# Kernel tuning notes

Measured on AMD Instinct MI355X. Metric: run time of the kernel, lower is better.

Reference implementation:

```python
import jax, jax.numpy as jnp
import numpy as np

B, C, H, N, M = 8, 256, 4, 2048, 2048
D = C // H  # head_dim = 64
EPS = 1e-5


def conv1d(x, W, b):
    # 1x1 Conv1d == per-position GEMM: x [B, Cin, N], W [Cout, Cin], b [Cout]
    return jnp.einsum('oi,bin->bon', W, x) + b[:, None]


def setup_inputs() -> dict:
    key = jax.random.key(0)
    ks = jax.random.split(key, 16)
    s = 1.0 / np.sqrt(C)
    s2 = 1.0 / np.sqrt(2 * C)
    return {
        'desc1': jax.random.normal(ks[0], (B, C, N), jnp.float32),
        'desc2': jax.random.normal(ks[1], (B, C, M), jnp.float32),
        'weight_v': jax.random.uniform(ks[2], (B, M), jnp.float32),
        'Wq': jax.random.normal(ks[3], (C, C), jnp.float32) * s,
        'bq': jnp.zeros((C,), jnp.float32),
        'Wk': jax.random.normal(ks[4], (C, C), jnp.float32) * s,
        'bk': jnp.zeros((C,), jnp.float32),
        'Wv': jax.random.normal(ks[5], (C, C), jnp.float32) * s,
        'bv': jnp.zeros((C,), jnp.float32),
        'Wm': jax.random.normal(ks[6], (C, C), jnp.float32) * s,
        'bm': jnp.zeros((C,), jnp.float32),
        'Wc1': jax.random.normal(ks[7], (2 * C, 2 * C), jnp.float32) * s2,
        'bc1': jnp.zeros((2 * C,), jnp.float32),
        'bn_gamma': jnp.ones((2 * C,), jnp.float32),
        'bn_beta': jnp.zeros((2 * C,), jnp.float32),
        'bn_mean': jnp.zeros((2 * C,), jnp.float32),
        'bn_var': jnp.ones((2 * C,), jnp.float32),
        'Wc2': jax.random.normal(ks[8], (C, 2 * C), jnp.float32) * s2,
        'bc2': jnp.zeros((C,), jnp.float32),
    }


def reference(desc1, desc2, weight_v, Wq, bq, Wk, bk, Wv, bv, Wm, bm,
              Wc1, bc1, bn_gamma, bn_beta, bn_mean, bn_var, Wc2, bc2):
    b = desc1.shape[0]
    # projections -> [B, H, D, N/M]
    q = conv1d(desc1, Wq, bq).reshape(b, H, D, -1)
    k = conv1d(desc2, Wk, bk).reshape(b, H, D, -1)
    v = conv1d(desc2, Wv, bv).reshape(b, H, D, -1)
    v = v * weight_v[:, None, None, :]
    score = jax.nn.softmax(jnp.einsum('bhdn,bhdm->bhnm', q, k) / jnp.sqrt(jnp.asarray(D, q.dtype)), axis=-1)
    add_value = jnp.einsum('bhnm,bhdm->bhdn', score, v).reshape(b, H * D, -1)
    add_value = conv1d(add_value, Wm, bm)
    cat = jnp.concatenate([desc1, add_value], axis=1)  # [B, 2C, N]
    h = conv1d(cat, Wc1, bc1)
    # BatchNorm (inference, running stats)
    inv = bn_gamma / jnp.sqrt(bn_var + EPS)
    h = jax.nn.relu(h * inv[:, None] + (bn_beta - bn_mean * inv)[:, None])
    return desc1 + conv1d(h, Wc2, bc2)
```

## Files before the change

### kernel.cpp

```cpp
#include <hip/hip_runtime.h>
#include <hip/hip_bf16.h>
#include <math.h>

constexpr int Bb = 8;
constexpr int Cc = 256;
constexpr int Hh = 4;
constexpr int Nn = 2048;
constexpr int Mm = 2048;
constexpr size_t BCN = (size_t)Bb * Cc * Nn;

typedef __attribute__((ext_vector_type(8))) short short8;
typedef __attribute__((ext_vector_type(4))) float f32x4;

__device__ __forceinline__ unsigned short bfu(float x) {
  __hip_bfloat16 b = __float2bfloat16(x);
  return __builtin_bit_cast(unsigned short, b);
}

__device__ __forceinline__ void gload16(const unsigned short* g, unsigned short* l) {
  __builtin_amdgcn_global_load_lds(
      (const __attribute__((address_space(1))) unsigned int*)g,
      (__attribute__((address_space(3))) unsigned int*)l, 16, 0, 0);
}

__global__ __launch_bounds__(256) void quantw_kernel(
    const float* __restrict__ s0, const float* __restrict__ s1,
    const float* __restrict__ s2, const float* __restrict__ s3,
    const float* __restrict__ s4, const float* __restrict__ s5,
    unsigned short* __restrict__ d0, unsigned short* __restrict__ d1,
    unsigned short* __restrict__ d2, unsigned short* __restrict__ d3,
    unsigned short* __restrict__ d4, unsigned short* __restrict__ d5)
{
  const int seg = blockIdx.y;
  const float* s; unsigned short* d; int cnt; float sc = 1.f;
  switch (seg) {
    case 0: s = s0; d = d0; cnt = 65536;  sc = 0.125f; break;
    case 1: s = s1; d = d1; cnt = 65536;  break;
    case 2: s = s2; d = d2; cnt = 65536;  break;
    case 3: s = s3; d = d3; cnt = 65536;  break;
    case 4: s = s4; d = d4; cnt = 262144; break;
    default: s = s5; d = d5; cnt = 131072; break;
  }
  for (int i = blockIdx.x * 256 + threadIdx.x; i < cnt / 4; i += 64 * 256) {
    float4 v = ((const float4*)s)[i];
    unsigned int lo = bfu(v.x * sc) | ((unsigned int)bfu(v.y * sc) << 16);
    unsigned int hi = bfu(v.z * sc) | ((unsigned int)bfu(v.w * sc) << 16);
    ((uint2*)d)[i] = make_uint2(lo, hi);
  }
}

__global__ __launch_bounds__(256) void trans_kernel(
    const float* __restrict__ S1, const float* __restrict__ S2,
    unsigned short* __restrict__ D1, unsigned short* __restrict__ D2)
{
  __shared__ float T[64][65];
  const int z = blockIdx.z, b = z & 7;
  const float* S = (z >> 3) ? S2 : S1;
  unsigned short* D = (z >> 3) ? D2 : D1;
  const int n0 = blockIdx.x * 64, c0 = blockIdx.y * 64;
  const int t = threadIdx.x, t4 = t >> 6, tl = t & 63;

  #pragma unroll
  for (int r = 0; r < 16; ++r) {
    int cl = r * 4 + t4;
    T[cl][tl] = S[((size_t)b * 256 + c0 + cl) * 2048 + n0 + tl];
  }
  __syncthreads();
  #pragma unroll
  for (int r = 0; r < 16; ++r) {
    int nl = r * 4 + t4;
    D[((size_t)b * 2048 + n0 + nl) * 256 + c0 + tl] = bfu(T[tl][nl]);
  }
}

template<int K1, int K2, int COUT, int EPI>
__global__ __launch_bounds__(256) void gemm_kernel(
    const unsigned short* __restrict__ Wb,
    const unsigned short* __restrict__ X1, const unsigned short* __restrict__ X2,
    const float* __restrict__ bias,
    const float* __restrict__ p0, const float* __restrict__ p1,
    const float* __restrict__ p2, const float* __restrict__ p3,
    void* __restrict__ Yv, float oscale)
{
  constexpr int KT = K1 + K2;
  constexpr bool TRANS = (EPI == 0 || EPI == 2 || EPI == 3);
  __shared__ unsigned short lds[2 * 128 * 64];
  unsigned short* Wl = lds;
  unsigned short* Xl = lds + 128 * 64;

  const int t = threadIdx.x;
  const int w = t >> 6, l = t & 63;
  const int c = l & 15, h4 = l >> 4;
  const int n0 = blockIdx.x * 128;
  const int o0 = blockIdx.y * 128;
  const int b  = blockIdx.z;
  const int wo = (w & 1) * 64, wn = (w >> 1) * 64;

  const int r8  = t >> 3;
  const int kgx = (t & 7) ^ (r8 & 7);

  const unsigned short* Xb1 = X1 + (size_t)b * 2048 * K1;

  f32x4 acc[4][4] = {};

  #pragma unroll 1
  for (int kt = 0; kt < KT / 64; ++kt) {
    __syncthreads();
    #pragma unroll
    for (int q = 0; q < 4; ++q) {
      int row = q * 32 + r8;
      gload16(Wb + (size_t)(o0 + row) * KT + kt * 64 + kgx * 8,
              Wl + q * 2048 + w * 512);
      const unsigned short* src;
      if constexpr (K2 == 0) {
        src = Xb1 + (size_t)(n0 + row) * K1 + kt * 64 + kgx * 8;
      } else {
        src = (kt * 64 < K1)
          ? Xb1 + (size_t)(n0 + row) * K1 + kt * 64 + kgx * 8
          : X2 + ((size_t)b * 2048 + n0 + row) * K2 + (kt * 64 - K1) + kgx * 8;
      }
      gload16(src, Xl + q * 2048 + w * 512);
    }
    __syncthreads();

    #pragma unroll
    for (int kk = 0; kk < 2; ++kk) {
      short8 wf[4], xf[4];
      #pragma unroll
      for (int f = 0; f < 4; ++f) {
        int row = wo + f * 16 + c;
        wf[f] = *(const short8*)((const char*)Wl + row * 128 + (((kk * 4 + h4) ^ (row & 7)) << 4));
      }
      #pragma unroll
      for (int f = 0; f < 4; ++f) {
        int row = wn + f * 16 + c;
        xf[f] = *(const short8*)((const char*)Xl + row * 128 + (((kk * 4 + h4) ^ (row & 7)) << 4));
      }
      #pragma unroll
      for (int i = 0; i < 4; ++i)
        #pragma unroll
        for (int j = 0; j < 4; ++j) {
          if constexpr (TRANS)
            acc[i][j] = __builtin_amdgcn_mfma_f32_16x16x32_bf16(xf[i], wf[j], acc[i][j], 0, 0, 0);
          else
            acc[i][j] = __builtin_amdgcn_mfma_f32_16x16x32_bf16(wf[i], xf[j], acc[i][j], 0, 0, 0);
        }
    }
  }

  if constexpr (EPI == 0) {
    unsigned short* Y = (unsigned short*)Yv;
    #pragma unroll
    for (int j = 0; j < 4; ++j) {
      int og = o0 + wo + j * 16 + c;
      float bb = bias[og] * oscale;
      int hh = og >> 6, d = og & 63;
      unsigned short* Yp = Y + (((size_t)b * Hh + hh) * 2048) * 64 + d;
      #pragma unroll
      for (int i = 0; i < 4; ++i) {
        #pragma unroll
        for (int r = 0; r < 4; ++r) {
          int ng = n0 + wn + i * 16 + h4 * 4 + r;
          Yp[(size_t)ng * 64] = bfu(acc[i][j][r] + bb);
        }
      }
    }
  } else if constexpr (EPI == 2) {
    unsigned short* Y = (unsigned short*)Yv;
    #pragma unroll
    for (int j = 0; j < 4; ++j) {
      int og = o0 + wo + j * 16 + c;
      float bb = bias[og];
      #pragma unroll
      for (int i = 0; i < 4; ++i)
        #pragma unroll
        for (int r = 0; r < 4; ++r) {
          int ng = n0 + wn + i * 16 + h4 * 4 + r;
          Y[((size_t)b * 2048 + ng) * 256 + og] = bfu(acc[i][j][r] + bb);
        }
    }
  } else if constexpr (EPI == 3) {
    unsigned short* Y = (unsigned short*)Yv;
    #pragma unroll
    for (int j = 0; j < 4; ++j) {
      int og = o0 + wo + j * 16 + c;
      float bb  = bias[og];
      float inv = p0[og] / sqrtf(p3[og] + 1e-5f);
      float add = p1[og] - p2[og] * inv;
      #pragma unroll
      for (int i = 0; i < 4; ++i)
        #pragma unroll
        for (int r = 0; r < 4; ++r) {
          int ng = n0 + wn + i * 16 + h4 * 4 + r;
          float v = fmaxf((acc[i][j][r] + bb) * inv + add, 0.f);
          Y[((size_t)b * 2048 + ng) * 512 + og] = bfu(v);
        }
    }
  } else if constexpr (EPI == 1) {
    unsigned short* Y = (unsigned short*)Yv;
    #pragma unroll
    for (int j = 0; j < 4; ++j) {
      int mg = n0 + wn + j * 16 + c;
      float sc = p0[(size_t)b * 2048 + mg];
      #pragma unroll
      for (int i = 0; i < 4; ++i)
        #pragma unroll
        for (int r = 0; r < 4; ++r) {
          int og = o0 + wo + i * 16 + h4 * 4 + r;
          Y[((size_t)b * 256 + og) * 2048 + mg] = bfu((acc[i][j][r] + bias[og]) * sc);
        }
    }
  } else {
    float* Y = (float*)Yv;
    #pragma unroll
    for (int j = 0; j < 4; ++j) {
      int ng = n0 + wn + j * 16 + c;
      #pragma unroll
      for (int i = 0; i < 4; ++i)
        #pragma unroll
        for (int r = 0; r < 4; ++r) {
          int og = o0 + wo + i * 16 + h4 * 4 + r;
          size_t idx = ((size_t)b * 256 + og) * 2048 + ng;
          Y[idx] = acc[i][j][r] + bias[og] + p0[idx];
        }
    }
  }
}

__global__ __launch_bounds__(256) void attn_mfma_kernel(
    const unsigned short* __restrict__ Qt, const unsigned short* __restrict__ Kt,
    const unsigned short* __restrict__ Vb, unsigned short* __restrict__ Ot)
{
  const int id  = blockIdx.x;
  const int xcd = id & 7;
  const int s8  = id >> 3;
  const int bh  = xcd + 8 * (s8 >> 4);
  const int nb  = s8 & 15;
  const int wv  = threadIdx.x >> 6;
  const int l   = threadIdx.x & 63;
  const int c   = l & 15;
  const int h   = l >> 4;
  const int n0  = nb * 128 + wv * 32;

  const unsigned short* Qw = Qt + ((size_t)bh * Nn + n0) * 64;
  const unsigned short* Kb = Kt + (size_t)bh * Mm * 64;
  const unsigned short* Vw = Vb + (size_t)bh * 64 * Mm;

  __shared__ unsigned short Pl[4][32 * 64];
  char* P = (char*)Pl[wv];

  short8 qf[2][2];
  #pragma unroll
  for (int j = 0; j < 2; ++j)
    #pragma unroll
    for (int ks = 0; ks < 2; ++ks)
      qf[j][ks] = *(const short8*)(Qw + ((size_t)(j*16 + c)) * 64 + ks*32 + h*8);

  f32x4 acc[4][2];
  #pragma unroll
  for (int d = 0; d < 4; ++d)
    #pragma unroll
    for (int j = 0; j < 2; ++j) acc[d][j] = (f32x4){0.f,0.f,0.f,0.f};
  float rowM[2] = {-1e30f, -1e30f};
  float rowL[2] = {0.f, 0.f};

  #pragma unroll 1
  for (int m0 = 0; m0 < Mm; m0 += 64) {
    short8 kf[4][2];
    #pragma unroll
    for (int g = 0; g < 4; ++g)
      #pragma unroll
      for (int ks = 0; ks < 2; ++ks)
        kf[g][ks] = *(const short8*)(Kb + ((size_t)(m0 + g*16 + c)) * 64 + ks*32 + h*8);

    f32x4 sc4[4][2];
    #pragma unroll
    for (int g = 0; g < 4; ++g)
      #pragma unroll
      for (int j = 0; j < 2; ++j) {
        f32x4 z = (f32x4){0.f,0.f,0.f,0.f};
        z = __builtin_amdgcn_mfma_f32_16x16x32_bf16(kf[g][0], qf[j][0], z, 0, 0, 0);
        z = __builtin_amdgcn_mfma_f32_16x16x32_bf16(kf[g][1], qf[j][1], z, 0, 0, 0);
        sc4[g][j] = z;
      }

    short8 vf[4][2];
    #pragma unroll
    for (int db = 0; db < 4; ++db)
      #pragma unroll
      for (int ks = 0; ks < 2; ++ks)
        vf[db][ks] = *(const short8*)(Vw + ((size_t)(db*16 + c)) * Mm + m0 + ks*32 + h*8);

    #pragma unroll
    for (int j = 0; j < 2; ++j) {
      float mx = -1e30f;
      #pragma unroll
      for (int g = 0; g < 4; ++g)
        #pragma unroll
        for (int r = 0; r < 4; ++r) mx = fmaxf(mx, sc4[g][j][r]);
      mx = fmaxf(mx, __shfl_xor(mx, 16));
      mx = fmaxf(mx, __shfl_xor(mx, 32));
      float nm = fmaxf(rowM[j], mx);
      float corr = __expf(rowM[j] - nm);
      rowM[j] = nm;
      float sum = 0.f;
      #pragma unroll
      for (int g = 0; g < 4; ++g) {
        #pragma unroll
        for (int r = 0; r < 4; ++r) {
          float e = __expf(sc4[g][j][r] - nm);
          sc4[g][j][r] = e;
          sum += e;
        }
      }
      sum += __shfl_xor(sum, 16);
      sum += __shfl_xor(sum, 32);
      rowL[j] = rowL[j] * corr + sum;
      #pragma unroll
      for (int db = 0; db < 4; ++db)
        #pragma unroll
        for (int r = 0; r < 4; ++r) acc[db][j][r] *= corr;

      #pragma unroll
      for (int g = 0; g < 4; ++g) {
        unsigned int lo = ((unsigned int)bfu(sc4[g][j][1]) << 16) | bfu(sc4[g][j][0]);
        unsigned int hi = ((unsigned int)bfu(sc4[g][j][3]) << 16) | bfu(sc4[g][j][2]);
        int off = (j*16 + c) * 128 + g*32 + h*8;
        off ^= (c & 7) << 4;
        *(uint2*)(P + off) = make_uint2(lo, hi);
      }
    }

    #pragma unroll
    for (int j = 0; j < 2; ++j) {
      short8 pf[2];
      #pragma unroll
      for (int ks = 0; ks < 2; ++ks) {
        int off = (j*16 + c) * 128 + ks*64 + h*16;
        off ^= (c & 7) << 4;
        pf[ks] = *(const short8*)(P + off);
      }
      #pragma unroll
      for (int db = 0; db < 4; ++db) {
        acc[db][j] = __builtin_amdgcn_mfma_f32_16x16x32_bf16(vf[db][0], pf[0], acc[db][j], 0, 0, 0);
        acc[db][j] = __builtin_amdgcn_mfma_f32_16x16x32_bf16(vf[db][1], pf[1], acc[db][j], 0, 0, 0);
      }
    }
  }

  const float invl[2] = {1.f / rowL[0], 1.f / rowL[1]};
  unsigned short* Ob = Ot + ((size_t)(bh >> 2) * Nn) * 256 + (bh & 3) * 64;
  #pragma unroll
  for (int db = 0; db < 4; ++db)
    #pragma unroll
    for (int j = 0; j < 2; ++j) {
      unsigned int lo = ((unsigned int)bfu(acc[db][j][1] * invl[j]) << 16) | bfu(acc[db][j][0] * invl[j]);
      unsigned int hi = ((unsigned int)bfu(acc[db][j][3] * invl[j]) << 16) | bfu(acc[db][j][2] * invl[j]);
      *(uint2*)(Ob + (size_t)(n0 + j*16 + c) * 256 + db*16 + h*4) = make_uint2(lo, hi);
    }
}

extern "C" void kernel_launch(void* const* d_in, const int* in_sizes, int n_in,
                              void* d_out, int out_size, void* d_ws, size_t ws_size,
                              hipStream_t stream)
{
  (void)in_sizes; (void)n_in; (void)out_size; (void)ws_size;
  const float* desc1 = (const float*)d_in[0];
  const float* desc2 = (const float*)d_in[1];
  const float* wvv   = (const float*)d_in[2];
  const float* Wq  = (const float*)d_in[3];  const float* bq  = (const float*)d_in[4];
  const float* Wk  = (const float*)d_in[5];  const float* bk  = (const float*)d_in[6];
  const float* Wv  = (const float*)d_in[7];  const float* bv  = (const float*)d_in[8];
  const float* Wm  = (const float*)d_in[9];  const float* bm  = (const float*)d_in[10];
  const float* Wc1 = (const float*)d_in[11]; const float* bc1 = (const float*)d_in[12];
  const float* bng = (const float*)d_in[13]; const float* bnb = (const float*)d_in[14];
  const float* bnm = (const float*)d_in[15]; const float* bnv = (const float*)d_in[16];
  const float* Wc2 = (const float*)d_in[17]; const float* bc2 = (const float*)d_in[18];
  float* out = (float*)d_out;

  unsigned short* u = (unsigned short*)d_ws;
  unsigned short* D1t  = u;
  unsigned short* D2t  = u + BCN;
  unsigned short* Qt   = u + 2 * BCN;
  unsigned short* Kt   = u + 3 * BCN;
  unsigned short* Vbb  = u + 4 * BCN;
  unsigned short* Ot    = D2t;
  unsigned short* MoutT = Qt;
  unsigned short* HT    = Kt;
  unsigned short* Wqb  = u + 5 * BCN;
  unsigned short* Wkb  = Wqb + 65536;
  unsigned short* Wvb  = Wkb + 65536;
  unsigned short* Wmb  = Wvb + 65536;
  unsigned short* Wc1b = Wmb + 65536;
  unsigned short* Wc2b = Wc1b + 262144;

  dim3 blk(256);
  quantw_kernel<<<dim3(64, 6), blk, 0, stream>>>(
      Wq, Wk, Wv, Wm, Wc1, Wc2, Wqb, Wkb, Wvb, Wmb, Wc1b, Wc2b);
  trans_kernel<<<dim3(32, 4, 16), blk, 0, stream>>>(desc1, desc2, D1t, D2t);

  gemm_kernel<256,0,256,0><<<dim3(16, 2, Bb), blk, 0, stream>>>(
      Wqb, D1t, nullptr, bq, nullptr,nullptr,nullptr,nullptr, Qt, 0.125f);
  gemm_kernel<256,0,256,0><<<dim3(16, 2, Bb), blk, 0, stream>>>(
      Wkb, D2t, nullptr, bk, nullptr,nullptr,nullptr,nullptr, Kt, 1.0f);
  gemm_kernel<256,0,256,1><<<dim3(16, 2, Bb), blk, 0, stream>>>(
      Wvb, D2t, nullptr, bv, wvv,nullptr,nullptr,nullptr, Vbb, 1.0f);
  attn_mfma_kernel<<<dim3(512), blk, 0, stream>>>(Qt, Kt, Vbb, Ot);
  gemm_kernel<256,0,256,2><<<dim3(16, 2, Bb), blk, 0, stream>>>(
      Wmb, Ot, nullptr, bm, nullptr,nullptr,nullptr,nullptr, MoutT, 1.0f);
  gemm_kernel<256,256,512,3><<<dim3(16, 4, Bb), blk, 0, stream>>>(
      Wc1b, D1t, MoutT, bc1, bng,bnb,bnm,bnv, HT, 1.0f);
  gemm_kernel<512,0,256,4><<<dim3(16, 2, Bb), blk, 0, stream>>>(
      Wc2b, HT, nullptr, bc2, desc1,nullptr,nullptr,nullptr, out, 1.0f);
}
```

Before: 299.3 us.

## Replace LDS-tiled GEMM with direct-load MFMA, add lazy-rescale exp2 softmax

The projection GEMMs drop LDS staging and double syncs. Each wave now loads its operand fragments straight from global memory into registers, with smaller 64x128 block tiles and twice as many blocks. The attention kernel switches to exp2 by folding log2(e) into the Q scale, and skips the running-max rescale when the new max exceeds the old by at most 8. It also raises wave priority around the MFMA blocks and unrolls the key loop by two. The GEMM change gives up LDS reuse across waves, so it adds global/L2 traffic in exchange for less synchronisation.

```diff
diff --git a/kernel.cpp b/kernel.cpp
--- a/kernel.cpp
+++ b/kernel.cpp
@@ -12,15 +12,11 @@
 typedef __attribute__((ext_vector_type(8))) short short8;
 typedef __attribute__((ext_vector_type(4))) float f32x4;
 
+constexpr float QSCALE = 0.125f * 1.4426950408889634f;
+
 __device__ __forceinline__ unsigned short bfu(float x) {
   __hip_bfloat16 b = __float2bfloat16(x);
   return __builtin_bit_cast(unsigned short, b);
-}
-
-__device__ __forceinline__ void gload16(const unsigned short* g, unsigned short* l) {
-  __builtin_amdgcn_global_load_lds(
-      (const __attribute__((address_space(1))) unsigned int*)g,
-      (__attribute__((address_space(3))) unsigned int*)l, 16, 0, 0);
 }
 
 __global__ __launch_bounds__(256) void quantw_kernel(
@@ -34,7 +30,7 @@
   const int seg = blockIdx.y;
   const float* s; unsigned short* d; int cnt; float sc = 1.f;
   switch (seg) {
-    case 0: s = s0; d = d0; cnt = 65536;  sc = 0.125f; break;
+    case 0: s = s0; d = d0; cnt = 65536;  sc = QSCALE; break;
     case 1: s = s1; d = d1; cnt = 65536;  break;
     case 2: s = s2; d = d2; cnt = 65536;  break;
     case 3: s = s3; d = d3; cnt = 65536;  break;
@@ -73,7 +69,7 @@
   }
 }
 
-template<int K1, int K2, int COUT, int EPI>
+template<int K1, int K2, int EPI>
 __global__ __launch_bounds__(256) void gemm_kernel(
     const unsigned short* __restrict__ Wb,
     const unsigned short* __restrict__ X1, const unsigned short* __restrict__ X2,
@@ -84,144 +80,116 @@
 {
   constexpr int KT = K1 + K2;
   constexpr bool TRANS = (EPI == 0 || EPI == 2 || EPI == 3);
-  __shared__ unsigned short lds[2 * 128 * 64];
-  unsigned short* Wl = lds;
-  unsigned short* Xl = lds + 128 * 64;
-
-  const int t = threadIdx.x;
-  const int w = t >> 6, l = t & 63;
-  const int c = l & 15, h4 = l >> 4;
-  const int n0 = blockIdx.x * 128;
-  const int o0 = blockIdx.y * 128;
+  const int t  = threadIdx.x;
+  const int wv = t >> 6, l = t & 63;
+  const int c  = l & 15, h4 = l >> 4;
+  const int n0 = blockIdx.x * 128 + wv * 32;
+  const int o0 = blockIdx.y * 64;
   const int b  = blockIdx.z;
-  const int wo = (w & 1) * 64, wn = (w >> 1) * 64;
-
-  const int r8  = t >> 3;
-  const int kgx = (t & 7) ^ (r8 & 7);
-
-  const unsigned short* Xb1 = X1 + (size_t)b * 2048 * K1;
-
-  f32x4 acc[4][4] = {};
-
-  #pragma unroll 1
-  for (int kt = 0; kt < KT / 64; ++kt) {
-    __syncthreads();
-    #pragma unroll
-    for (int q = 0; q < 4; ++q) {
-      int row = q * 32 + r8;
-      gload16(Wb + (size_t)(o0 + row) * KT + kt * 64 + kgx * 8,
-              Wl + q * 2048 + w * 512);
-      const unsigned short* src;
-      if constexpr (K2 == 0) {
-        src = Xb1 + (size_t)(n0 + row) * K1 + kt * 64 + kgx * 8;
-      } else {
-        src = (kt * 64 < K1)
-          ? Xb1 + (size_t)(n0 + row) * K1 + kt * 64 + kgx * 8
-          : X2 + ((size_t)b * 2048 + n0 + row) * K2 + (kt * 64 - K1) + kgx * 8;
-      }
-      gload16(src, Xl + q * 2048 + w * 512);
-    }
-    __syncthreads();
-
-    #pragma unroll
-    for (int kk = 0; kk < 2; ++kk) {
-      short8 wf[4], xf[4];
+
+  f32x4 acc[2][4] = {};
+
+  #pragma unroll 4
+  for (int kt = 0; kt < KT / 32; ++kt) {
+    const int k0 = kt * 32 + h4 * 8;
+    const unsigned short* xb; int xs;
+    if constexpr (K2 == 0) {
+      xb = X1 + ((size_t)b * 2048 + n0) * K1 + k0; xs = K1;
+    } else {
+      if (kt * 32 < K1) { xb = X1 + ((size_t)b * 2048 + n0) * K1 + k0; xs = K1; }
+      else              { xb = X2 + ((size_t)b * 2048 + n0) * K2 + (k0 - K1); xs = K2; }
+    }
+    short8 xf[2], wf[4];
+    #pragma unroll
+    for (int j = 0; j < 2; ++j)
+      xf[j] = *(const short8*)(xb + (size_t)(j * 16 + c) * xs);
+    #pragma unroll
+    for (int f = 0; f < 4; ++f)
+      wf[f] = *(const short8*)(Wb + (size_t)(o0 + f * 16 + c) * KT + k0);
+    __builtin_amdgcn_s_setprio(1);
+    #pragma unroll
+    for (int j = 0; j < 2; ++j)
       #pragma unroll
       for (int f = 0; f < 4; ++f) {
-        int row = wo + f * 16 + c;
-        wf[f] = *(const short8*)((const char*)Wl + row * 128 + (((kk * 4 + h4) ^ (row & 7)) << 4));
-      }
-      #pragma unroll
-      for (int f = 0; f < 4; ++f) {
-        int row = wn + f * 16 + c;
-        xf[f] = *(const short8*)((const char*)Xl + row * 128 + (((kk * 4 + h4) ^ (row & 7)) << 4));
-      }
-      #pragma unroll
-      for (int i = 0; i < 4; ++i)
-        #pragma unroll
-        for (int j = 0; j < 4; ++j) {
-          if constexpr (TRANS)
-            acc[i][j] = __builtin_amdgcn_mfma_f32_16x16x32_bf16(xf[i], wf[j], acc[i][j], 0, 0, 0);
-          else
-            acc[i][j] = __builtin_amdgcn_mfma_f32_16x16x32_bf16(wf[i], xf[j], acc[i][j], 0, 0, 0);
-        }
-    }
+        if constexpr (TRANS)
+          acc[j][f] = __builtin_amdgcn_mfma_f32_16x16x32_bf16(xf[j], wf[f], acc[j][f], 0, 0, 0);
+        else
+          acc[j][f] = __builtin_amdgcn_mfma_f32_16x16x32_bf16(wf[f], xf[j], acc[j][f], 0, 0, 0);
+      }
+    __builtin_amdgcn_s_setprio(0);
   }
 
   if constexpr (EPI == 0) {
     unsigned short* Y = (unsigned short*)Yv;
-    #pragma unroll
-    for (int j = 0; j < 4; ++j) {
-      int og = o0 + wo + j * 16 + c;
-      float bb = bias[og] * oscale;
-      int hh = og >> 6, d = og & 63;
-      unsigned short* Yp = Y + (((size_t)b * Hh + hh) * 2048) * 64 + d;
-      #pragma unroll
-      for (int i = 0; i < 4; ++i) {
+    const int by = blockIdx.y;
+    #pragma unroll
+    for (int f = 0; f < 4; ++f) {
+      float bb = bias[o0 + f * 16 + c] * oscale;
+      #pragma unroll
+      for (int j = 0; j < 2; ++j)
         #pragma unroll
         for (int r = 0; r < 4; ++r) {
-          int ng = n0 + wn + i * 16 + h4 * 4 + r;
-          Yp[(size_t)ng * 64] = bfu(acc[i][j][r] + bb);
+          int n = n0 + j * 16 + h4 * 4 + r;
+          Y[(((size_t)b * Hh + by) * 2048 + n) * 64 + f * 16 + c] = bfu(acc[j][f][r] + bb);
         }
-      }
     }
   } else if constexpr (EPI == 2) {
     unsigned short* Y = (unsigned short*)Yv;
     #pragma unroll
-    for (int j = 0; j < 4; ++j) {
-      int og = o0 + wo + j * 16 + c;
-      float bb = bias[og];
-      #pragma unroll
-      for (int i = 0; i < 4; ++i)
+    for (int f = 0; f < 4; ++f) {
+      int o = o0 + f * 16 + c;
+      float bb = bias[o];
+      #pragma unroll
+      for (int j = 0; j < 2; ++j)
         #pragma unroll
         for (int r = 0; r < 4; ++r) {
-          int ng = n0 + wn + i * 16 + h4 * 4 + r;
-          Y[((size_t)b * 2048 + ng) * 256 + og] = bfu(acc[i][j][r] + bb);
+          int n = n0 + j * 16 + h4 * 4 + r;
+          Y[((size_t)b * 2048 + n) * 256 + o] = bfu(acc[j][f][r] + bb);
         }
     }
   } else if constexpr (EPI == 3) {
     unsigned short* Y = (unsigned short*)Yv;
     #pragma unroll
-    for (int j = 0; j < 4; ++j) {
-      int og = o0 + wo + j * 16 + c;
-      float bb  = bias[og];
-      float inv = p0[og] / sqrtf(p3[og] + 1e-5f);
-      float add = p1[og] - p2[og] * inv;
-      #pragma unroll
-      for (int i = 0; i < 4; ++i)
+    for (int f = 0; f < 4; ++f) {
+      int o = o0 + f * 16 + c;
+      float bb  = bias[o];
+      float inv = p0[o] / sqrtf(p3[o] + 1e-5f);
+      float add = p1[o] - p2[o] * inv;
+      #pragma unroll
+      for (int j = 0; j < 2; ++j)
         #pragma unroll
         for (int r = 0; r < 4; ++r) {
-          int ng = n0 + wn + i * 16 + h4 * 4 + r;
-          float v = fmaxf((acc[i][j][r] + bb) * inv + add, 0.f);
-          Y[((size_t)b * 2048 + ng) * 512 + og] = bfu(v);
+          int n = n0 + j * 16 + h4 * 4 + r;
+          float v = fmaxf((acc[j][f][r] + bb) * inv + add, 0.f);
+          Y[((size_t)b * 2048 + n) * 512 + o] = bfu(v);
         }
     }
   } else if constexpr (EPI == 1) {
     unsigned short* Y = (unsigned short*)Yv;
     #pragma unroll
-    for (int j = 0; j < 4; ++j) {
-      int mg = n0 + wn + j * 16 + c;
-      float sc = p0[(size_t)b * 2048 + mg];
-      #pragma unroll
-      for (int i = 0; i < 4; ++i)
+    for (int j = 0; j < 2; ++j) {
+      int m = n0 + j * 16 + c;
+      float sc = p0[(size_t)b * 2048 + m];
+      #pragma unroll
+      for (int f = 0; f < 4; ++f)
         #pragma unroll
         for (int r = 0; r < 4; ++r) {
-          int og = o0 + wo + i * 16 + h4 * 4 + r;
-          Y[((size_t)b * 256 + og) * 2048 + mg] = bfu((acc[i][j][r] + bias[og]) * sc);
+          int o = o0 + f * 16 + h4 * 4 + r;
+          Y[((size_t)b * 256 + o) * 2048 + m] = bfu((acc[j][f][r] + bias[o]) * sc);
         }
     }
   } else {
     float* Y = (float*)Yv;
     #pragma unroll
-    for (int j = 0; j < 4; ++j) {
-      int ng = n0 + wn + j * 16 + c;
-      #pragma unroll
-      for (int i = 0; i < 4; ++i)
+    for (int j = 0; j < 2; ++j) {
+      int n = n0 + j * 16 + c;
+      #pragma unroll
+      for (int f = 0; f < 4; ++f)
         #pragma unroll
         for (int r = 0; r < 4; ++r) {
-          int og = o0 + wo + i * 16 + h4 * 4 + r;
-          size_t idx = ((size_t)b * 256 + og) * 2048 + ng;
-          Y[idx] = acc[i][j][r] + bias[og] + p0[idx];
+          int o = o0 + f * 16 + h4 * 4 + r;
+          size_t idx = ((size_t)b * 256 + o) * 2048 + n;
+          Y[idx] = acc[j][f][r] + bias[o] + p0[idx];
         }
     }
   }
@@ -264,7 +232,7 @@
   float rowM[2] = {-1e30f, -1e30f};
   float rowL[2] = {0.f, 0.f};
 
-  #pragma unroll 1
+  #pragma unroll 2
   for (int m0 = 0; m0 < Mm; m0 += 64) {
     short8 kf[4][2];
     #pragma unroll
@@ -274,6 +242,7 @@
         kf[g][ks] = *(const short8*)(Kb + ((size_t)(m0 + g*16 + c)) * 64 + ks*32 + h*8);
 
     f32x4 sc4[4][2];
+    __builtin_amdgcn_s_setprio(1);
     #pragma unroll
     for (int g = 0; g < 4; ++g)
       #pragma unroll
@@ -283,6 +252,7 @@
         z = __builtin_amdgcn_mfma_f32_16x16x32_bf16(kf[g][1], qf[j][1], z, 0, 0, 0);
         sc4[g][j] = z;
       }
+    __builtin_amdgcn_s_setprio(0);
 
     short8 vf[4][2];
     #pragma unroll
@@ -300,26 +270,40 @@
         for (int r = 0; r < 4; ++r) mx = fmaxf(mx, sc4[g][j][r]);
       mx = fmaxf(mx, __shfl_xor(mx, 16));
       mx = fmaxf(mx, __shfl_xor(mx, 32));
-      float nm = fmaxf(rowM[j], mx);
-      float corr = __expf(rowM[j] - nm);
-      rowM[j] = nm;
+
       float sum = 0.f;
-      #pragma unroll
-      for (int g = 0; g < 4; ++g) {
-        #pragma unroll
-        for (int r = 0; r < 4; ++r) {
-          float e = __expf(sc4[g][j][r] - nm);
-          sc4[g][j][r] = e;
-          sum += e;
-        }
-      }
-      sum += __shfl_xor(sum, 16);
-      sum += __shfl_xor(sum, 32);
-      rowL[j] = rowL[j] * corr + sum;
-      #pragma unroll
-      for (int db = 0; db < 4; ++db)
-        #pragma unroll
-        for (int r = 0; r < 4; ++r) acc[db][j][r] *= corr;
+      if (__all(mx - rowM[j] <= 8.f)) {
+        #pragma unroll
+        for (int g = 0; g < 4; ++g)
+          #pragma unroll
+          for (int r = 0; r < 4; ++r) {
+            float e = exp2f(sc4[g][j][r] - rowM[j]);
+            sc4[g][j][r] = e;
+            sum += e;
+          }
+        sum += __shfl_xor(sum, 16);
+        sum += __shfl_xor(sum, 32);
+        rowL[j] += sum;
+      } else {
+        float nm = fmaxf(rowM[j], mx);
+        float corr = exp2f(rowM[j] - nm);
+        rowM[j] = nm;
+        #pragma unroll
+        for (int g = 0; g < 4; ++g)
+          #pragma unroll
+          for (int r = 0; r < 4; ++r) {
+            float e = exp2f(sc4[g][j][r] - nm);
+            sc4[g][j][r] = e;
+            sum += e;
+          }
+        sum += __shfl_xor(sum, 16);
+        sum += __shfl_xor(sum, 32);
+        rowL[j] = rowL[j] * corr + sum;
+        #pragma unroll
+        for (int db = 0; db < 4; ++db)
+          #pragma unroll
+          for (int r = 0; r < 4; ++r) acc[db][j][r] *= corr;
+      }
 
       #pragma unroll
       for (int g = 0; g < 4; ++g) {
@@ -340,11 +324,13 @@
         off ^= (c & 7) << 4;
         pf[ks] = *(const short8*)(P + off);
       }
+      __builtin_amdgcn_s_setprio(1);
       #pragma unroll
       for (int db = 0; db < 4; ++db) {
         acc[db][j] = __builtin_amdgcn_mfma_f32_16x16x32_bf16(vf[db][0], pf[0], acc[db][j], 0, 0, 0);
         acc[db][j] = __builtin_amdgcn_mfma_f32_16x16x32_bf16(vf[db][1], pf[1], acc[db][j], 0, 0, 0);
       }
+      __builtin_amdgcn_s_setprio(0);
     }
   }
 
@@ -399,17 +385,17 @@
       Wq, Wk, Wv, Wm, Wc1, Wc2, Wqb, Wkb, Wvb, Wmb, Wc1b, Wc2b);
   trans_kernel<<<dim3(32, 4, 16), blk, 0, stream>>>(desc1, desc2, D1t, D2t);
 
-  gemm_kernel<256,0,256,0><<<dim3(16, 2, Bb), blk, 0, stream>>>(
-      Wqb, D1t, nullptr, bq, nullptr,nullptr,nullptr,nullptr, Qt, 0.125f);
-  gemm_kernel<256,0,256,0><<<dim3(16, 2, Bb), blk, 0, stream>>>(
+  gemm_kernel<256,0,0><<<dim3(16, 4, Bb), blk, 0, stream>>>(
+      Wqb, D1t, nullptr, bq, nullptr,nullptr,nullptr,nullptr, Qt, QSCALE);
+  gemm_kernel<256,0,0><<<dim3(16, 4, Bb), blk, 0, stream>>>(
       Wkb, D2t, nullptr, bk, nullptr,nullptr,nullptr,nullptr, Kt, 1.0f);
-  gemm_kernel<256,0,256,1><<<dim3(16, 2, Bb), blk, 0, stream>>>(
+  gemm_kernel<256,0,1><<<dim3(16, 4, Bb), blk, 0, stream>>>(
       Wvb, D2t, nullptr, bv, wvv,nullptr,nullptr,nullptr, Vbb, 1.0f);
   attn_mfma_kernel<<<dim3(512), blk, 0, stream>>>(Qt, Kt, Vbb, Ot);
-  gemm_kernel<256,0,256,2><<<dim3(16, 2, Bb), blk, 0, stream>>>(
+  gemm_kernel<256,0,2><<<dim3(16, 4, Bb), blk, 0, stream>>>(
       Wmb, Ot, nullptr, bm, nullptr,nullptr,nullptr,nullptr, MoutT, 1.0f);
-  gemm_kernel<256,256,512,3><<<dim3(16, 4, Bb), blk, 0, stream>>>(
+  gemm_kernel<256,256,3><<<dim3(16, 8, Bb), blk, 0, stream>>>(
       Wc1b, D1t, MoutT, bc1, bng,bnb,bnm,bnv, HT, 1.0f);
-  gemm_kernel<512,0,256,4><<<dim3(16, 2, Bb), blk, 0, stream>>>(
+  gemm_kernel<512,0,4><<<dim3(16, 4, Bb), blk, 0, stream>>>(
       Wc2b, HT, nullptr, bc2, desc1,nullptr,nullptr,nullptr, out, 1.0f);
 }
```

New measurement: 365.5 us. 22.1% more time.
